# Performance work log

Hardware: AMD Instinct MI355X
Metric: run time of the kernel (lower is better)

## Reference

```python
import jax, jax.numpy as jnp
import numpy as np

N, F_IN, F_OUT = 8192, 256, 256
ALPHA = 0.2  # LeakyReLU negative slope
NEG = -9e15

def setup_inputs() -> dict:
    key = jax.random.key(0)
    k1, k2, k3, k4, k5 = jax.random.split(key, 5)
    h = jax.random.normal(k1, (N, F_IN), dtype=jnp.float32)
    adj = jax.random.randint(k2, (N, N), 0, 2, dtype=jnp.int32)
    W_w = jax.random.normal(k3, (F_IN, F_OUT), dtype=jnp.float32) / np.sqrt(F_IN)
    W_b = jax.random.normal(k4, (F_OUT,), dtype=jnp.float32) * 0.01
    a = jax.random.normal(k5, (2 * F_OUT, 1), dtype=jnp.float32) / np.sqrt(2 * F_OUT)
    return {"h": h, "adj": adj, "W_w": W_w, "W_b": W_b, "a": a}

def reference(h, adj, W_w, W_b, a):
    # Wh: [N, F_OUT]
    Wh = h @ W_w + W_b
    a1 = a[:F_OUT, 0]   # scores for source node i (row)
    a2 = a[F_OUT:, 0]   # scores for target node j (col)
    # e[i,j] = leakyrelu(Wh_i . a1 + Wh_j . a2)  -- separable form of the
    # original repeat/cat construction, identical math without the NxNx2F tensor.
    e = jax.nn.leaky_relu((Wh @ a1)[:, None] + (Wh @ a2)[None, :], negative_slope=ALPHA)
    attention = jnp.where(adj > 0, e, NEG)
    attention = jax.nn.softmax(attention, axis=1)
    # dropout is identity in eval / p=0
    h_prime = attention @ Wh  # [N, F_OUT]
    return h_prime
```

## Files before the change

### kernel.cpp

```cpp
#include <hip/hip_runtime.h>
#include <stdint.h>

#define NN 8192
#define FD 256
#define LOG2E 1.44269504088896340736f
#define SPLIT 4
#define JSLICE (NN / SPLIT)
#define NIT (JSLICE / 32)

typedef __attribute__((ext_vector_type(8))) __bf16 bf16x8;
typedef __attribute__((ext_vector_type(4))) float f32x4;

__device__ __forceinline__ unsigned short f2bf(float x) {
    unsigned u = __float_as_uint(x);
    u = u + 0x7fffu + ((u >> 16) & 1u);
    return (unsigned short)(u >> 16);
}
__device__ __forceinline__ bf16x8 ld_bf8(const unsigned short* p) {
    uint4 v = *(const uint4*)p;
    return __builtin_bit_cast(bf16x8, v);
}
__device__ __forceinline__ unsigned pack_trunc2(float a, float b) {
    return __builtin_amdgcn_perm(__float_as_uint(b), __float_as_uint(a), 0x07060302u);
}

__global__ __launch_bounds__(256) void wtrans_kernel(const float* __restrict__ W,
                                                     unsigned short* __restrict__ WbT) {
    int idx = blockIdx.x * 256 + threadIdx.x;
    int k = idx >> 8, f = idx & 255;
    WbT[f * 256 + k] = f2bf(W[idx]);
}

__global__ __launch_bounds__(256) void adjpack_kernel(const int* __restrict__ adj,
                                                      unsigned* __restrict__ adjB) {
    int t = threadIdx.x;
    int l = t & 63, w = t >> 6;
    int i = blockIdx.x * 4 + w;
    const int* arow = adj + (size_t)i * NN;
    unsigned* brow = adjB + (size_t)i * (NN / 32);
    #pragma unroll 2
    for (int c = 0; c < 32; ++c) {
        int base = c * 256;
        int v0 = arow[base + l];
        int v1 = arow[base + 64 + l];
        int v2 = arow[base + 128 + l];
        int v3 = arow[base + 192 + l];
        unsigned long long b0 = __ballot(v0 > 0);
        unsigned long long b1 = __ballot(v1 > 0);
        unsigned long long b2 = __ballot(v2 > 0);
        unsigned long long b3 = __ballot(v3 > 0);
        if (l == 0) {
            uint4 lo = make_uint4((unsigned)b0, (unsigned)(b0 >> 32),
                                  (unsigned)b1, (unsigned)(b1 >> 32));
            uint4 hi = make_uint4((unsigned)b2, (unsigned)(b2 >> 32),
                                  (unsigned)b3, (unsigned)(b3 >> 32));
            *(uint4*)(brow + c * 8) = lo;
            *(uint4*)(brow + c * 8 + 4) = hi;
        }
    }
}

__global__ __launch_bounds__(256) void gemm1_kernel(const float* __restrict__ h,
                                                    const unsigned short* __restrict__ WbT,
                                                    const float* __restrict__ bias,
                                                    const float* __restrict__ av,
                                                    unsigned short* __restrict__ PBu,
                                                    float* __restrict__ f1p,
                                                    float* __restrict__ f2p) {
    __shared__ float Wh_s[256 * 33];
    __shared__ float red_s[2 * 8 * 32];
    int t = threadIdx.x;
    int l = t & 63, w = t >> 6;
    int i0 = blockIdx.x * 32;
    int fbase = w * 64;
    int cl = l & 15, q = l >> 4;

    f32x4 acc[2][4] = {};
    const float* hA0 = h + (size_t)(i0 + cl) * FD;
    const float* hA1 = h + (size_t)(i0 + 16 + cl) * FD;

    #pragma unroll
    for (int ks = 0; ks < 8; ++ks) {
        int kk = ks * 32 + q * 8;
        union { unsigned short u[8]; bf16x8 v; } ua0, ua1;
        float4 x0 = *(const float4*)(hA0 + kk);
        float4 x1 = *(const float4*)(hA0 + kk + 4);
        float4 y0 = *(const float4*)(hA1 + kk);
        float4 y1 = *(const float4*)(hA1 + kk + 4);
        ua0.u[0]=f2bf(x0.x); ua0.u[1]=f2bf(x0.y); ua0.u[2]=f2bf(x0.z); ua0.u[3]=f2bf(x0.w);
        ua0.u[4]=f2bf(x1.x); ua0.u[5]=f2bf(x1.y); ua0.u[6]=f2bf(x1.z); ua0.u[7]=f2bf(x1.w);
        ua1.u[0]=f2bf(y0.x); ua1.u[1]=f2bf(y0.y); ua1.u[2]=f2bf(y0.z); ua1.u[3]=f2bf(y0.w);
        ua1.u[4]=f2bf(y1.x); ua1.u[5]=f2bf(y1.y); ua1.u[6]=f2bf(y1.z); ua1.u[7]=f2bf(y1.w);
        #pragma unroll
        for (int bg = 0; bg < 4; ++bg) {
            bf16x8 bF = ld_bf8(WbT + (fbase + bg * 16 + cl) * 256 + kk);
            acc[0][bg] = __builtin_amdgcn_mfma_f32_16x16x32_bf16(ua0.v, bF, acc[0][bg], 0, 0, 0);
            acc[1][bg] = __builtin_amdgcn_mfma_f32_16x16x32_bf16(ua1.v, bF, acc[1][bg], 0, 0, 0);
        }
    }

    #pragma unroll
    for (int mt = 0; mt < 2; ++mt)
        #pragma unroll
        for (int bg = 0; bg < 4; ++bg)
            #pragma unroll
            for (int e = 0; e < 4; ++e) {
                int il = mt * 16 + q * 4 + e;
                int fl = fbase + bg * 16 + cl;
                Wh_s[fl * 33 + il] = acc[mt][bg][e] + bias[fl];
            }
    __syncthreads();
    {
        size_t jcBase = (size_t)blockIdx.x * 8192;
        #pragma unroll
        for (int u = 0; u < 4; ++u) {
            int fg = u * 4 + (t >> 6);
            int ll = t & 63;
            int c2 = ll & 15, q2 = ll >> 4;
            const float* src = &Wh_s[(fg * 16 + c2) * 33 + q2 * 8];
            union { unsigned short us[8]; uint4 v; } p;
            #pragma unroll
            for (int e = 0; e < 8; ++e) p.us[e] = f2bf(src[e]);
            *(uint4*)(PBu + jcBase + fg * 512 + ll * 8) = p.v;
        }
    }
    {
        int i = t & 31, fc = t >> 5;
        float s1 = 0.f, s2 = 0.f;
        #pragma unroll
        for (int fo = 0; fo < 32; ++fo) {
            int f = fc * 32 + fo;
            float wv = Wh_s[f * 33 + i];
            s1 += wv * av[f];
            s2 += wv * av[256 + f];
        }
        red_s[fc * 32 + i] = s1;
        red_s[256 + fc * 32 + i] = s2;
    }
    __syncthreads();
    if (t < 32) {
        float s = 0.f;
        #pragma unroll
        for (int fc = 0; fc < 8; ++fc) s += red_s[fc * 32 + t];
        f1p[i0 + t] = s * LOG2E;
    } else if (t < 64) {
        int i = t - 32;
        float s = 0.f;
        #pragma unroll
        for (int fc = 0; fc < 8; ++fc) s += red_s[256 + fc * 32 + i];
        f2p[i0 + i] = s * LOG2E;
    }
}

__global__ __launch_bounds__(256) void gat_kernel(const unsigned* __restrict__ adjB,
                                                  const unsigned short* __restrict__ PBu,
                                                  const float* __restrict__ f1p,
                                                  const float* __restrict__ f2p,
                                                  float* __restrict__ num,
                                                  float* __restrict__ den) {
    int t = threadIdx.x;
    int l = t & 63, w = t >> 6;
    int strip = blockIdx.x & 127;
    int s = blockIdx.x >> 7;
    int i0 = strip * 64 + w * 16;
    int j0 = s * JSLICE;
    int cl = l & 15, q = l >> 4;

    float f1v = f1p[i0 + cl];
    const unsigned* mrow = adjB + (size_t)(i0 + cl) * (NN / 32) + j0 / 32;
    const float* f2r = f2p + j0 + q * 8;
    const unsigned short* pb = PBu + (size_t)(j0 / 32) * 8192 + l * 8;

    f32x4 acc[16] = {};
    float rs = 0.f;

    #pragma unroll 1
    for (int jt = 0; jt < NIT; ++jt) {
        unsigned mw = mrow[jt];
        float4 F0 = *(const float4*)(f2r + jt * 32);
        float4 F1 = *(const float4*)(f2r + jt * 32 + 4);
        bf16x8 B[16];
        const unsigned short* pbj = pb + (size_t)jt * 8192;
        #pragma unroll
        for (int fg = 0; fg < 16; ++fg) B[fg] = ld_bf8(pbj + fg * 512);

        unsigned bits = mw >> (q * 8);
        float fe[8] = {F0.x, F0.y, F0.z, F0.w, F1.x, F1.y, F1.z, F1.w};
        float wv[8];
        #pragma unroll
        for (int e = 0; e < 8; ++e) {
            float sv = f1v + fe[e];
            sv = fmaxf(sv, 0.2f * sv);
            float x = __builtin_amdgcn_exp2f(sv);
            x = (bits >> e) & 1 ? x : 0.f;
            rs += x;
            wv[e] = x;
        }
        union { unsigned u[4]; bf16x8 v; } af;
        af.u[0] = pack_trunc2(wv[0], wv[1]);
        af.u[1] = pack_trunc2(wv[2], wv[3]);
        af.u[2] = pack_trunc2(wv[4], wv[5]);
        af.u[3] = pack_trunc2(wv[6], wv[7]);

        #pragma unroll
        for (int fg = 0; fg < 16; ++fg)
            acc[fg] = __builtin_amdgcn_mfma_f32_16x16x32_bf16(af.v, B[fg], acc[fg], 0, 0, 0);
    }

    rs += __shfl_xor(rs, 16);
    rs += __shfl_xor(rs, 32);
    if (l < 16) den[(size_t)s * NN + i0 + l] = rs;

    float* nrow = num + (size_t)s * NN * FD;
    #pragma unroll
    for (int e = 0; e < 4; ++e) {
        int r = i0 + q * 4 + e;
        #pragma unroll
        for (int fg = 0; fg < 16; ++fg)
            nrow[(size_t)r * FD + fg * 16 + cl] = acc[fg][e];
    }
}

__global__ __launch_bounds__(256) void combine_kernel(const float* __restrict__ num,
                                                      const float* __restrict__ den,
                                                      float* __restrict__ out) {
    int idx = blockIdx.x * 256 + threadIdx.x;
    int i = idx >> 8;
    float nsum = 0.f, dsum = 0.f;
    #pragma unroll
    for (int s = 0; s < SPLIT; ++s) {
        nsum += num[(size_t)s * NN * FD + idx];
        dsum += den[(size_t)s * NN + i];
    }
    out[idx] = nsum / dsum;
}

extern "C" void kernel_launch(void* const* d_in, const int* in_sizes, int n_in,
                              void* d_out, int out_size, void* d_ws, size_t ws_size,
                              hipStream_t stream) {
    const float* h   = (const float*)d_in[0];
    const int*   adj = (const int*)d_in[1];
    const float* W   = (const float*)d_in[2];
    const float* b   = (const float*)d_in[3];
    const float* a   = (const float*)d_in[4];
    float* out = (float*)d_out;

    char* ws = (char*)d_ws;
    unsigned short* PBu = (unsigned short*)ws;
    unsigned short* WbT = (unsigned short*)(ws + (4u << 20));
    float* f1p = (float*)(ws + (4u << 20) + (128u << 10));
    float* f2p = f1p + NN;
    float* den = f2p + NN;
    unsigned* adjB = (unsigned*)(ws + (8u << 20));
    float* num = (float*)(ws + (16u << 20));

    adjpack_kernel<<<NN / 4, 256, 0, stream>>>(adj, adjB);
    wtrans_kernel<<<256, 256, 0, stream>>>(W, WbT);
    gemm1_kernel<<<256, 256, 0, stream>>>(h, WbT, b, a, PBu, f1p, f2p);
    gat_kernel<<<128 * SPLIT, 256, 0, stream>>>(adjB, PBu, f1p, f2p, num, den);
    combine_kernel<<<NN * FD / 256, 256, 0, stream>>>(num, den, out);
}
```

Measured before the change: 489.2 us.

## Double rows per wave in GAT kernel, stage transposed mask and f2 in LDS

Each wave now computes two 16-row tiles that share the same loaded P·Wh B fragments, halving the B-operand global traffic per output row. The packed adjacency bitmask is transposed by a new kernel so a block can load its mask words coalesced into shared memory, and f2 is staged in LDS. SPLIT goes from 4 to 8 to keep enough blocks, which doubles the partial num buffer written to and read back by the combine kernel. It also raises register pressure, since accumulators double to 32 MFMA tiles under launch bounds of 2 blocks per CU.

```diff
diff --git a/kernel.cpp b/kernel.cpp
--- a/kernel.cpp
+++ b/kernel.cpp
@@ -4,7 +4,7 @@
 #define NN 8192
 #define FD 256
 #define LOG2E 1.44269504088896340736f
-#define SPLIT 4
+#define SPLIT 8
 #define JSLICE (NN / SPLIT)
 #define NIT (JSLICE / 32)
 
@@ -60,6 +60,26 @@
     }
 }
 
+__global__ __launch_bounds__(256) void btrans_kernel(const unsigned* __restrict__ rm,
+                                                     unsigned* __restrict__ tm) {
+    __shared__ unsigned tile[64 * 65];
+    int t = threadIdx.x;
+    int l = t & 63, r0 = t >> 6;
+    int i0 = (blockIdx.x & 127) * 64;
+    int w0 = (blockIdx.x >> 7) * 64;
+    #pragma unroll
+    for (int k = 0; k < 16; ++k) {
+        int r = k * 4 + r0;
+        tile[r * 65 + l] = rm[(size_t)(i0 + r) * (NN / 32) + w0 + l];
+    }
+    __syncthreads();
+    #pragma unroll
+    for (int k = 0; k < 16; ++k) {
+        int wi = k * 4 + r0;
+        tm[(size_t)(w0 + wi) * NN + i0 + l] = tile[l * 65 + wi];
+    }
+}
+
 __global__ __launch_bounds__(256) void gemm1_kernel(const float* __restrict__ h,
                                                     const unsigned short* __restrict__ WbT,
                                                     const float* __restrict__ bias,
@@ -152,72 +172,98 @@
     }
 }
 
-__global__ __launch_bounds__(256) void gat_kernel(const unsigned* __restrict__ adjB,
-                                                  const unsigned short* __restrict__ PBu,
-                                                  const float* __restrict__ f1p,
-                                                  const float* __restrict__ f2p,
-                                                  float* __restrict__ num,
-                                                  float* __restrict__ den) {
+__global__ __launch_bounds__(256, 2) void gat_kernel(const unsigned* __restrict__ adjBT,
+                                                     const unsigned short* __restrict__ PBu,
+                                                     const float* __restrict__ f1p,
+                                                     const float* __restrict__ f2p,
+                                                     float* __restrict__ num,
+                                                     float* __restrict__ den) {
+    __shared__ unsigned mask_s[NIT * 128];
+    __shared__ float f2_s[JSLICE];
+
     int t = threadIdx.x;
     int l = t & 63, w = t >> 6;
-    int strip = blockIdx.x & 127;
-    int s = blockIdx.x >> 7;
-    int i0 = strip * 64 + w * 16;
+    int strip = blockIdx.x & 63;
+    int s = blockIdx.x >> 6;
+    int i0b = strip * 128;
     int j0 = s * JSLICE;
+    int jw0 = j0 / 32;
     int cl = l & 15, q = l >> 4;
 
-    float f1v = f1p[i0 + cl];
-    const unsigned* mrow = adjB + (size_t)(i0 + cl) * (NN / 32) + j0 / 32;
-    const float* f2r = f2p + j0 + q * 8;
-    const unsigned short* pb = PBu + (size_t)(j0 / 32) * 8192 + l * 8;
-
-    f32x4 acc[16] = {};
-    float rs = 0.f;
+    #pragma unroll
+    for (int c = 0; c < 16; ++c) {
+        int idx = c * 256 + t;
+        int jt = idx >> 7, rl = idx & 127;
+        mask_s[idx] = adjBT[(size_t)(jw0 + jt) * NN + i0b + rl];
+    }
+    *(float4*)&f2_s[t * 4] = *(const float4*)(f2p + j0 + t * 4);
+    __syncthreads();
+
+    int rA = w * 32 + cl;
+    float f1vA = f1p[i0b + rA];
+    float f1vB = f1p[i0b + rA + 16];
+    const unsigned short* pb = PBu + (size_t)jw0 * 8192 + l * 8;
+
+    f32x4 accA[16] = {}, accB[16] = {};
+    float rsA = 0.f, rsB = 0.f;
 
     #pragma unroll 1
     for (int jt = 0; jt < NIT; ++jt) {
-        unsigned mw = mrow[jt];
-        float4 F0 = *(const float4*)(f2r + jt * 32);
-        float4 F1 = *(const float4*)(f2r + jt * 32 + 4);
         bf16x8 B[16];
         const unsigned short* pbj = pb + (size_t)jt * 8192;
         #pragma unroll
         for (int fg = 0; fg < 16; ++fg) B[fg] = ld_bf8(pbj + fg * 512);
 
-        unsigned bits = mw >> (q * 8);
+        unsigned mwA = mask_s[jt * 128 + rA];
+        unsigned mwB = mask_s[jt * 128 + rA + 16];
+        float4 F0 = *(const float4*)&f2_s[jt * 32 + q * 8];
+        float4 F1 = *(const float4*)&f2_s[jt * 32 + q * 8 + 4];
+
+        unsigned bA = mwA >> (q * 8), bB = mwB >> (q * 8);
         float fe[8] = {F0.x, F0.y, F0.z, F0.w, F1.x, F1.y, F1.z, F1.w};
-        float wv[8];
+        float wA[8], wB[8];
         #pragma unroll
         for (int e = 0; e < 8; ++e) {
-            float sv = f1v + fe[e];
-            sv = fmaxf(sv, 0.2f * sv);
-            float x = __builtin_amdgcn_exp2f(sv);
-            x = (bits >> e) & 1 ? x : 0.f;
-            rs += x;
-            wv[e] = x;
-        }
-        union { unsigned u[4]; bf16x8 v; } af;
-        af.u[0] = pack_trunc2(wv[0], wv[1]);
-        af.u[1] = pack_trunc2(wv[2], wv[3]);
-        af.u[2] = pack_trunc2(wv[4], wv[5]);
-        af.u[3] = pack_trunc2(wv[6], wv[7]);
-
-        #pragma unroll
-        for (int fg = 0; fg < 16; ++fg)
-            acc[fg] = __builtin_amdgcn_mfma_f32_16x16x32_bf16(af.v, B[fg], acc[fg], 0, 0, 0);
-    }
-
-    rs += __shfl_xor(rs, 16);
-    rs += __shfl_xor(rs, 32);
-    if (l < 16) den[(size_t)s * NN + i0 + l] = rs;
+            float sA = f1vA + fe[e];
+            sA = fmaxf(sA, 0.2f * sA);
+            float xA = __builtin_amdgcn_exp2f(sA);
+            xA = (bA >> e) & 1 ? xA : 0.f;
+            rsA += xA; wA[e] = xA;
+            float sB = f1vB + fe[e];
+            sB = fmaxf(sB, 0.2f * sB);
+            float xB = __builtin_amdgcn_exp2f(sB);
+            xB = (bB >> e) & 1 ? xB : 0.f;
+            rsB += xB; wB[e] = xB;
+        }
+        union { unsigned u[4]; bf16x8 v; } afA, afB;
+        afA.u[0] = pack_trunc2(wA[0], wA[1]); afA.u[1] = pack_trunc2(wA[2], wA[3]);
+        afA.u[2] = pack_trunc2(wA[4], wA[5]); afA.u[3] = pack_trunc2(wA[6], wA[7]);
+        afB.u[0] = pack_trunc2(wB[0], wB[1]); afB.u[1] = pack_trunc2(wB[2], wB[3]);
+        afB.u[2] = pack_trunc2(wB[4], wB[5]); afB.u[3] = pack_trunc2(wB[6], wB[7]);
+
+        #pragma unroll
+        for (int fg = 0; fg < 16; ++fg) {
+            accA[fg] = __builtin_amdgcn_mfma_f32_16x16x32_bf16(afA.v, B[fg], accA[fg], 0, 0, 0);
+            accB[fg] = __builtin_amdgcn_mfma_f32_16x16x32_bf16(afB.v, B[fg], accB[fg], 0, 0, 0);
+        }
+    }
+
+    rsA += __shfl_xor(rsA, 16); rsA += __shfl_xor(rsA, 32);
+    rsB += __shfl_xor(rsB, 16); rsB += __shfl_xor(rsB, 32);
+    if (l < 16) {
+        den[(size_t)s * NN + i0b + w * 32 + l] = rsA;
+        den[(size_t)s * NN + i0b + w * 32 + 16 + l] = rsB;
+    }
 
     float* nrow = num + (size_t)s * NN * FD;
     #pragma unroll
     for (int e = 0; e < 4; ++e) {
-        int r = i0 + q * 4 + e;
-        #pragma unroll
-        for (int fg = 0; fg < 16; ++fg)
-            nrow[(size_t)r * FD + fg * 16 + cl] = acc[fg][e];
+        int r0 = i0b + w * 32 + q * 4 + e;
+        #pragma unroll
+        for (int fg = 0; fg < 16; ++fg) {
+            nrow[(size_t)r0 * FD + fg * 16 + cl] = accA[fg][e];
+            nrow[(size_t)(r0 + 16) * FD + fg * 16 + cl] = accB[fg][e];
+        }
     }
 }
 
@@ -251,12 +297,14 @@
     float* f1p = (float*)(ws + (4u << 20) + (128u << 10));
     float* f2p = f1p + NN;
     float* den = f2p + NN;
-    unsigned* adjB = (unsigned*)(ws + (8u << 20));
-    float* num = (float*)(ws + (16u << 20));
+    unsigned* adjB  = (unsigned*)(ws + (8u << 20));
+    unsigned* adjBT = (unsigned*)(ws + (16u << 20));
+    float* num = (float*)(ws + (24u << 20));
 
     adjpack_kernel<<<NN / 4, 256, 0, stream>>>(adj, adjB);
     wtrans_kernel<<<256, 256, 0, stream>>>(W, WbT);
+    btrans_kernel<<<512, 256, 0, stream>>>(adjB, adjBT);
     gemm1_kernel<<<256, 256, 0, stream>>>(h, WbT, b, a, PBu, f1p, f2p);
-    gat_kernel<<<128 * SPLIT, 256, 0, stream>>>(adjB, PBu, f1p, f2p, num, den);
+    gat_kernel<<<64 * SPLIT, 256, 0, stream>>>(adjBT, PBu, f1p, f2p, num, den);
     combine_kernel<<<NN * FD / 256, 256, 0, stream>>>(num, den, out);
 }
```

Result: no change. 485.7 us (-0.7%).
